# Optimization experiments

Measured on AMD Instinct MI355X. Metric: run time of the kernel, lower is better.

## Reference

```python
import jax, jax.numpy as jnp
import numpy as np

ROUTINGS = 3

def squash(x):
    # x: [..., O]; squash along last dim
    norm = jnp.linalg.norm(x, axis=-1, keepdims=True)
    scale = norm ** 2 / (1 + norm ** 2) / (norm + 1e-9)
    return scale * x

def setup_inputs() -> dict:
    key = jax.random.key(0)
    k1, k2 = jax.random.split(key)
    B, K, I, O, C = 256, 10, 1152, 16, 8
    x = jax.random.normal(k1, (B, I, C), dtype=jnp.float32)
    w = jax.random.normal(k2, (K, I, O, C), dtype=jnp.float32) * 0.05
    return {"x": x, "w": w}

def reference(x, w):
    # x: [B, I, Cin], w: [K, I, O, Cin]
    # u_hat[b,k,i,o] = sum_c w[k,i,o,c] * x[b,i,c]
    u_hat = jnp.einsum('kioc,bic->bkio', w, x)  # [B, K, I, O]
    B, K, I, O = u_hat.shape
    b = jnp.zeros((B, K, I, 1), dtype=u_hat.dtype)
    # routing iterations (fixed small loop); intermediate iters use detached u_hat
    u_hat_d = jax.lax.stop_gradient(u_hat)
    for _ in range(ROUTINGS - 1):
        c = jax.nn.softmax(b, axis=1)              # softmax over output capsules K
        s = jnp.sum(c * u_hat_d, axis=2)           # [B, K, O]
        v = squash(s)                              # [B, K, O]
        uv = jnp.einsum('bkio,bko->bki', u_hat_d, v)[..., None]  # [B, K, I, 1]
        b = b + uv
    c = jax.nn.softmax(b, axis=1)
    s = jnp.sum(c * u_hat, axis=2)
    v = squash(s)
    return v  # [B, K, O]
```

## Files before the change

### kernel.cpp

```cpp
#include <hip/hip_runtime.h>

#define B_ 256
#define K_ 10
#define I_ 1152
#define O_ 16
#define C_ 8
#define BKO (B_*K_*O_)
#define NX 72

static __device__ __forceinline__ unsigned short f32_bf16(float f) {
    unsigned int u = __float_as_uint(f);
    u += 0x7FFFu + ((u >> 16) & 1u);
    return (unsigned short)(u >> 16);
}

template <int CTRL>
static __device__ __forceinline__ float dpp_add(float v) {
    int x = __builtin_amdgcn_update_dpp(0, __float_as_int(v), CTRL, 0xF, 0xF, true);
    return v + __int_as_float(x);
}
static __device__ __forceinline__ float row16_sum(float v) {
    v = dpp_add<0xB1>(v);
    v = dpp_add<0x4E>(v);
    v = dpp_add<0x141>(v);
    v = dpp_add<0x140>(v);
    return v;
}
static __device__ __forceinline__ float quad4_sum(float v) {
    v = dpp_add<0xB1>(v);
    v = dpp_add<0x4E>(v);
    return v;
}

__global__ __launch_bounds__(256) void uhat_kernel(
    const float* __restrict__ x, const float* __restrict__ w,
    unsigned short* __restrict__ u, float* __restrict__ part)
{
    __shared__ float w_lds[16 * 132];
    __shared__ float p_lds[64 * 17];
    const int t   = threadIdx.x;
    const int i_l = t & 15, tg = t >> 4;
    const int i0  = blockIdx.x * 16;
    const int b0  = blockIdx.y * 64 + tg * 4;
    const int k   = blockIdx.z;
    const int i   = i0 + i_l;
    const bool row_leader = (i_l == 0);

    float4 xr[4][2];
#pragma unroll
    for (int bb = 0; bb < 4; bb++) {
        const float4* xp = (const float4*)(x + ((size_t)(b0 + bb) * I_ + i) * C_);
        xr[bb][0] = xp[0];
        xr[bb][1] = xp[1];
    }

    {
        const float4* ws = (const float4*)(w + ((size_t)k * I_ + i0) * O_ * C_);
#pragma unroll
        for (int r = 0; r < 2; r++) {
            int idx = r * 256 + t;
            int ii = idx >> 5, rem = idx & 31;
            *(float4*)&w_lds[ii * 132 + rem * 4] = ws[idx];
        }
    }
    __syncthreads();

    unsigned int pk[4][8];
#pragma unroll
    for (int oo = 0; oo < 8; oo++) {
        float d[4][2];
#pragma unroll
        for (int h = 0; h < 2; h++) {
            const int o = oo * 2 + h;
            const float4 w0 = *(const float4*)&w_lds[i_l * 132 + o * 8];
            const float4 w1 = *(const float4*)&w_lds[i_l * 132 + o * 8 + 4];
#pragma unroll
            for (int bb = 0; bb < 4; bb++) {
                d[bb][h] = w0.x*xr[bb][0].x + w0.y*xr[bb][0].y
                         + w0.z*xr[bb][0].z + w0.w*xr[bb][0].w
                         + w1.x*xr[bb][1].x + w1.y*xr[bb][1].y
                         + w1.z*xr[bb][1].z + w1.w*xr[bb][1].w;
            }
        }
#pragma unroll
        for (int bb = 0; bb < 4; bb++) {
#pragma unroll
            for (int h = 0; h < 2; h++) {
                const float rs = row16_sum(d[bb][h]);
                if (row_leader)
                    p_lds[(tg * 4 + bb) * 17 + oo * 2 + h] = rs;
            }
        }
#pragma unroll
        for (int bb = 0; bb < 4; bb++)
            pk[bb][oo] = (unsigned int)f32_bf16(d[bb][0]) |
                         ((unsigned int)f32_bf16(d[bb][1]) << 16);
    }
#pragma unroll
    for (int bb = 0; bb < 4; bb++) {
        unsigned int* dst = (unsigned int*)
            (u + (((size_t)(b0 + bb) * K_ + k) * I_ + i) * O_);
        *(uint4*)(dst)     = make_uint4(pk[bb][0], pk[bb][1], pk[bb][2], pk[bb][3]);
        *(uint4*)(dst + 4) = make_uint4(pk[bb][4], pk[bb][5], pk[bb][6], pk[bb][7]);
    }

    __syncthreads();
    {
        const int bl = t >> 2, o4 = (t & 3) * 4;
        float4 v;
        v.x = p_lds[bl * 17 + o4 + 0];
        v.y = p_lds[bl * 17 + o4 + 1];
        v.z = p_lds[bl * 17 + o4 + 2];
        v.w = p_lds[bl * 17 + o4 + 3];
        *(float4*)&part[(((size_t)blockIdx.x * K_ + k) * 256
                         + blockIdx.y * 64 + bl) * O_ + o4] = v;
    }
}

static __device__ __forceinline__ void sweep(
    const unsigned short* __restrict__ ub, int i_l,
    const float* __restrict__ v_lds, int og, float acc[K_][4])
{
#pragma unroll
    for (int k = 0; k < K_; k++)
#pragma unroll
        for (int j = 0; j < 4; j++) acc[k][j] = 0.f;

    uint2 P[K_], Q[K_];
#pragma unroll
    for (int k = 0; k < K_; k++)
        P[k] = *(const uint2*)(ub + ((size_t)k * I_ + i_l) * O_);

#pragma unroll 1
    for (int ic = 0; ic < 9; ic++) {
        if (ic + 1 < 9) {
            const int i = (ic + 1) * 128 + i_l;
#pragma unroll
            for (int k = 0; k < K_; k++)
                Q[k] = *(const uint2*)(ub + ((size_t)k * I_ + i) * O_);
        }
        float c[K_];
        float Z = 0.f;
#pragma unroll
        for (int k = 0; k < K_; k++) {
            const float f0 = __uint_as_float(P[k].x << 16);
            const float f1 = __uint_as_float(P[k].x & 0xffff0000u);
            const float f2 = __uint_as_float(P[k].y << 16);
            const float f3 = __uint_as_float(P[k].y & 0xffff0000u);
            const float* vk = &v_lds[k * 16 + og * 4];
            float lk = f0 * vk[0] + f1 * vk[1] + f2 * vk[2] + f3 * vk[3];
            lk = quad4_sum(lk);
            c[k] = __expf(lk);
            Z += c[k];
        }
        const float inv = 1.0f / Z;
#pragma unroll
        for (int k = 0; k < K_; k++) {
            const float ck = c[k] * inv;
            acc[k][0] = fmaf(ck, __uint_as_float(P[k].x << 16),        acc[k][0]);
            acc[k][1] = fmaf(ck, __uint_as_float(P[k].x & 0xffff0000u), acc[k][1]);
            acc[k][2] = fmaf(ck, __uint_as_float(P[k].y << 16),        acc[k][2]);
            acc[k][3] = fmaf(ck, __uint_as_float(P[k].y & 0xffff0000u), acc[k][3]);
        }
#pragma unroll
        for (int k = 0; k < K_; k++) P[k] = Q[k];
    }
}

static __device__ __forceinline__ void block_reduce(
    float acc[K_][4], float* __restrict__ red, int lane, int wv)
{
#pragma unroll
    for (int k = 0; k < K_; k++)
#pragma unroll
        for (int j = 0; j < 4; j++) {
            float a = acc[k][j];
            a += __shfl_xor(a, 4);  a += __shfl_xor(a, 8);
            a += __shfl_xor(a, 16); a += __shfl_xor(a, 32);
            acc[k][j] = a;
        }
    if (lane < 4) {
#pragma unroll
        for (int k = 0; k < K_; k++)
            *(float4*)&red[wv * 160 + k * 16 + lane * 4] =
                make_float4(acc[k][0], acc[k][1], acc[k][2], acc[k][3]);
    }
    __syncthreads();
}

static __device__ __forceinline__ float sum8(const float* __restrict__ red, int t)
{
    float s = 0.f;
#pragma unroll
    for (int wgi = 0; wgi < 8; wgi++) s += red[wgi * 160 + t];
    return s;
}

static __device__ __forceinline__ float squash_v(float s) {
    float n2 = s * s;
    n2 += __shfl_xor(n2, 1); n2 += __shfl_xor(n2, 2);
    n2 += __shfl_xor(n2, 4); n2 += __shfl_xor(n2, 8);
    const float norm = sqrtf(n2);
    return s * (n2 / (1.0f + n2) / (norm + 1e-9f));
}

__global__ __launch_bounds__(512) void route_all(
    const unsigned short* __restrict__ u, const float* __restrict__ part,
    float* __restrict__ out)
{
    __shared__ float red[8 * 160];
    __shared__ float v_lds[160];
    __shared__ float v1_lds[160];

    const int t    = threadIdx.x;
    const int og   = t & 3, i_l = t >> 2;
    const int b    = blockIdx.x;
    const int lane = t & 63, wv = t >> 6;

    const unsigned short* ub = u + (size_t)b * K_ * I_ * O_ + og * 4;
    float acc[K_][4];

    if (t < 160) {
        const int k = t >> 4, o = t & 15;
        const float* pb = part + ((size_t)k * 256 + b) * O_ + o;
        float s = 0.f;
#pragma unroll
        for (int xb = 0; xb < NX; xb++)
            s += pb[(size_t)xb * BKO];
        float v = squash_v(s * (1.0f / K_));
        v1_lds[t] = v;
        v_lds[t]  = v;
    }
    __syncthreads();

    sweep(ub, i_l, v_lds, og, acc);
    block_reduce(acc, red, lane, wv);
    float v12 = 0.f;
    if (t < 160) v12 = v1_lds[t] + squash_v(sum8(red, t));
    __syncthreads();
    if (t < 160) v_lds[t] = v12;
    __syncthreads();

    sweep(ub, i_l, v_lds, og, acc);
    block_reduce(acc, red, lane, wv);
    if (t < 160)
        out[(size_t)b * 160 + t] = squash_v(sum8(red, t));
}

extern "C" void kernel_launch(void* const* d_in, const int* in_sizes, int n_in,
                              void* d_out, int out_size, void* d_ws, size_t ws_size,
                              hipStream_t stream)
{
    const float* x = (const float*)d_in[0];
    const float* w = (const float*)d_in[1];
    float* outp = (float*)d_out;

    float* part = (float*)d_ws;
    unsigned short* u = (unsigned short*)(part + (size_t)NX * BKO);

    uhat_kernel<<<dim3(72, 4, 10), 256, 0, stream>>>(x, w, u, part);
    route_all<<<B_, 512, 0, stream>>>(u, part, outp);
}
```

Before: 123.5 us.

## Double-buffer u_hat chunks into LDS via global_load_lds in routing sweep

The routing sweep no longer prefetches each thread's u_hat slice into registers. Instead, all waves cooperatively stage each 128-capsule chunk into a double-buffered LDS array using direct global-to-LDS loads, and threads read their values from LDS. This is meant to turn per-thread 8-byte loads into wide 16-byte async transfers that overlap with compute, and to free registers held by the prefetch. In exchange it uses about 80KB of shared memory per block and adds a block-wide barrier per chunk.

```diff
diff --git a/kernel.cpp b/kernel.cpp
--- a/kernel.cpp
+++ b/kernel.cpp
@@ -117,28 +117,49 @@
     }
 }
 
+static __device__ __forceinline__ void stage(
+    const unsigned short* __restrict__ ub0, int ic,
+    unsigned short* __restrict__ buf, int wv, int lane)
+{
+#pragma unroll
+    for (int j = 0; j < 5; j++) {
+        const int r = wv * 5 + j;
+        const int k = r >> 2, q = r & 3;
+        const unsigned short* gp =
+            ub0 + ((size_t)k * I_ + ic * 128 + q * 32) * O_ + lane * 8;
+        unsigned short* lp = buf + r * 512;
+        __builtin_amdgcn_global_load_lds(
+            (const __attribute__((address_space(1))) void*)gp,
+            (__attribute__((address_space(3))) void*)lp,
+            16, 0, 0);
+    }
+}
+
 static __device__ __forceinline__ void sweep(
-    const unsigned short* __restrict__ ub, int i_l,
-    const float* __restrict__ v_lds, int og, float acc[K_][4])
+    const unsigned short* __restrict__ ub0,
+    unsigned short (*__restrict__ ubuf)[20480],
+    const float* __restrict__ v_lds,
+    int i_l, int og, int wv, int lane, float acc[K_][4])
 {
 #pragma unroll
     for (int k = 0; k < K_; k++)
 #pragma unroll
         for (int j = 0; j < 4; j++) acc[k][j] = 0.f;
 
-    uint2 P[K_], Q[K_];
-#pragma unroll
-    for (int k = 0; k < K_; k++)
-        P[k] = *(const uint2*)(ub + ((size_t)k * I_ + i_l) * O_);
+    stage(ub0, 0, ubuf[0], wv, lane);
+    __syncthreads();
 
 #pragma unroll 1
     for (int ic = 0; ic < 9; ic++) {
-        if (ic + 1 < 9) {
-            const int i = (ic + 1) * 128 + i_l;
-#pragma unroll
-            for (int k = 0; k < K_; k++)
-                Q[k] = *(const uint2*)(ub + ((size_t)k * I_ + i) * O_);
-        }
+        if (ic + 1 < 9)
+            stage(ub0, ic + 1, ubuf[(ic + 1) & 1], wv, lane);
+
+        const unsigned short* bp = ubuf[ic & 1] + i_l * 16 + og * 4;
+        uint2 P[K_];
+#pragma unroll
+        for (int k = 0; k < K_; k++)
+            P[k] = *(const uint2*)(bp + k * 2048);
+
         float c[K_];
         float Z = 0.f;
 #pragma unroll
@@ -157,13 +178,12 @@
 #pragma unroll
         for (int k = 0; k < K_; k++) {
             const float ck = c[k] * inv;
-            acc[k][0] = fmaf(ck, __uint_as_float(P[k].x << 16),        acc[k][0]);
+            acc[k][0] = fmaf(ck, __uint_as_float(P[k].x << 16),         acc[k][0]);
             acc[k][1] = fmaf(ck, __uint_as_float(P[k].x & 0xffff0000u), acc[k][1]);
-            acc[k][2] = fmaf(ck, __uint_as_float(P[k].y << 16),        acc[k][2]);
+            acc[k][2] = fmaf(ck, __uint_as_float(P[k].y << 16),         acc[k][2]);
             acc[k][3] = fmaf(ck, __uint_as_float(P[k].y & 0xffff0000u), acc[k][3]);
         }
-#pragma unroll
-        for (int k = 0; k < K_; k++) P[k] = Q[k];
+        __syncthreads();
     }
 }
 
@@ -208,6 +228,7 @@
     const unsigned short* __restrict__ u, const float* __restrict__ part,
     float* __restrict__ out)
 {
+    __shared__ unsigned short ubuf[2][20480];
     __shared__ float red[8 * 160];
     __shared__ float v_lds[160];
     __shared__ float v1_lds[160];
@@ -217,7 +238,7 @@
     const int b    = blockIdx.x;
     const int lane = t & 63, wv = t >> 6;
 
-    const unsigned short* ub = u + (size_t)b * K_ * I_ * O_ + og * 4;
+    const unsigned short* ub0 = u + (size_t)b * K_ * I_ * O_;
     float acc[K_][4];
 
     if (t < 160) {
@@ -233,7 +254,7 @@
     }
     __syncthreads();
 
-    sweep(ub, i_l, v_lds, og, acc);
+    sweep(ub0, ubuf, v_lds, i_l, og, wv, lane, acc);
     block_reduce(acc, red, lane, wv);
     float v12 = 0.f;
     if (t < 160) v12 = v1_lds[t] + squash_v(sum8(red, t));
@@ -241,7 +262,7 @@
     if (t < 160) v_lds[t] = v12;
     __syncthreads();
 
-    sweep(ub, i_l, v_lds, og, acc);
+    sweep(ub0, ubuf, v_lds, i_l, og, wv, lane, acc);
     block_reduce(acc, red, lane, wv);
     if (t < 160)
         out[(size_t)b * 160 + t] = squash_v(sum8(red, t));
```

Measured after the change: 126.6 us. +2.5%, slower.
